# Kernel optimization log

Hardware: AMD Instinct MI355X
Metric: run time of the kernel (lower is better)

The kernel has to match this reference:

```python
import jax, jax.numpy as jnp
import numpy as np

B, T, V, D = 256, 128, 32000, 512
DT = 0.04
CUBIC = 0.008
LAMBDA = 0.1
SIGNAL_SCALE = 0.5
NORM_EPS = 1e-8       # state_norm_eps
SIG_EPS = 1e-6        # signal_eps
SLOW_DECAY = 0.05
SLOW_LR = 0.05
W_FAST = 1.0
W_SLOW = 0.3
CONV_STEPS = 4
LN_EPS = 1e-5


def make_diffusion_matrix(dim):
    rng = np.random.default_rng(42)
    q, _ = np.linalg.qr(rng.standard_normal((dim, dim)).astype(np.float64))
    u = rng.random(dim)
    eig = -0.2 - (0.05 + 0.3 * u)
    return jnp.asarray((q * eig) @ q.T, dtype=jnp.float32)


def setup_inputs() -> dict:
    key = jax.random.key(0)
    k1, k2, k3 = jax.random.split(key, 3)
    tokens = jax.random.randint(k1, (B, T), 0, V)
    embed = jax.random.normal(k2, (V, D), dtype=jnp.float32) * 0.02
    readout_w = jax.random.normal(k3, (V, D), dtype=jnp.float32) * 0.02
    diffusion = make_diffusion_matrix(D)
    gamma = jnp.float32(0.2)
    beta = jnp.float32(0.75)
    return {"tokens": tokens, "embed": embed, "readout_w": readout_w,
            "diffusion": diffusion, "gamma": gamma, "beta": beta}


def _layernorm(x):
    mu = jnp.mean(x, axis=-1, keepdims=True)
    var = jnp.mean((x - mu) ** 2, axis=-1, keepdims=True)
    return (x - mu) / jnp.sqrt(var + LN_EPS)


def _norm(x):
    return jnp.linalg.norm(x, axis=-1, keepdims=True)


def _context_vector(fast, slow):
    combined = W_FAST * fast + W_SLOW * slow
    fn = _norm(fast)
    cn = _norm(combined)
    fast_dir = fast / (fn + SIG_EPS)
    comb_dir = combined / (cn + SIG_EPS)
    return jnp.where(fn > 1e-8, fast_dir,
                     jnp.where(cn > 1e-8, comb_dir, jnp.zeros_like(fast)))


def _step_state(state, signal, diffusion, beta):
    c = state - jnp.mean(state, axis=-1, keepdims=True)
    drift = (state @ diffusion.T + CUBIC * jnp.tanh(c)
             + beta * (SIGNAL_SCALE * signal) - LAMBDA * state)
    s = state + DT * drift
    s = jnp.nan_to_num(s, nan=0.0, posinf=0.0, neginf=0.0)
    s = s / (_norm(s) + NORM_EPS)
    return jnp.clip(s, -10.0, 10.0)


def reference(tokens, embed, readout_w, diffusion, gamma, beta):
    # tokens: [B,T] int; states: [B,D]
    fast0 = jnp.zeros((tokens.shape[0], D), dtype=embed.dtype)
    slow0 = jnp.zeros_like(fast0)

    def token_step(carry, tok):
        fast, slow = carry
        emb = _layernorm(embed[tok])                       # [B,D]
        base = emb / jnp.maximum(_norm(emb), 1e-12)
        ctx = _context_vector(fast, slow)
        sig = base + gamma * ctx
        sig = sig / (_norm(sig) + SIG_EPS)
        for _ in range(CONV_STEPS):
            fast = _step_state(fast, sig, diffusion, beta)
        slow = (1.0 - SLOW_DECAY) * slow + SLOW_LR * fast
        sn = _norm(slow)
        slow = jnp.where(sn > 0.5, slow * (0.5 / (sn + 1e-12)), slow)
        return (fast, slow), None

    (fast, slow), _ = jax.lax.scan(token_step, (fast0, slow0), tokens.T)
    combined = W_FAST * fast + W_SLOW * slow               # [B,D]
    logits = combined @ readout_w.T                        # [B,V]
    return logits
```

## Files before the change

### kernel.cpp

```cpp
#include <hip/hip_runtime.h>
#include <math.h>

#define DDIM 512
#define TLEN 128
#define RB   8
#define NWG  32
#define VDIM 32000
#define NWAVE 8
#define SR   528

typedef _Float16 f16x8 __attribute__((ext_vector_type(8)));
typedef float    f32x4 __attribute__((ext_vector_type(4)));
typedef _Float16 h2    __attribute__((ext_vector_type(2)));

__device__ __forceinline__ unsigned int pkh2(float a, float b) {
  h2 v; v.x = (_Float16)a; v.y = (_Float16)b;
  return __builtin_bit_cast(unsigned int, v);
}
__device__ __forceinline__ float h2f(unsigned short h) {
  return (float)__builtin_bit_cast(_Float16, h);
}
__device__ __forceinline__ unsigned short f2h(float f) {
  return __builtin_bit_cast(unsigned short, (_Float16)f);
}
__device__ __forceinline__ float tanh_fast(float x) {
#if __has_builtin(__builtin_amdgcn_exp2f) && __has_builtin(__builtin_amdgcn_rcpf)
  const float e = __builtin_amdgcn_exp2f(x * 2.885390081777927f);
  return 1.f - 2.f * __builtin_amdgcn_rcpf(e + 1.f);
#else
  const float e = exp2f(x * 2.885390081777927f);
  return 1.f - 2.f / (e + 1.f);
#endif
}
__device__ __forceinline__ f32x4 unpk4(uint2 u) {
  f32x4 r;
  r[0] = h2f((unsigned short)(u.x & 0xffff));
  r[1] = h2f((unsigned short)(u.x >> 16));
  r[2] = h2f((unsigned short)(u.y & 0xffff));
  r[3] = h2f((unsigned short)(u.y >> 16));
  return r;
}

__device__ __forceinline__ void wg_barrier() {
  asm volatile("s_waitcnt lgkmcnt(0)" ::: "memory");
  __builtin_amdgcn_s_barrier();
  asm volatile("" ::: "memory");
}

__global__ __launch_bounds__(256) void pack_diffusion(
    const float* __restrict__ A, uint4* __restrict__ pk)
{
  const int slot = blockIdx.x * 256 + threadIdx.x;
  const int l  = slot & 63;
  const int fr = slot >> 6;
  const int kt = fr & 15;
  const int it = fr >> 4;
  const float* src = A + (size_t)(it * 16 + (l & 15)) * DDIM + kt * 32 + (l >> 4) * 8;
  pk[slot] = make_uint4(pkh2(src[0], src[1]), pkh2(src[2], src[3]),
                        pkh2(src[4], src[5]), pkh2(src[6], src[7]));
}

__global__ __launch_bounds__(512) void precompute_mubi(
    const int*   __restrict__ tokens,
    const float* __restrict__ embed,
    float4*      __restrict__ mubi)
{
  const int idx = blockIdx.x * 8 + (threadIdx.x >> 6);
  const int l   = threadIdx.x & 63;
  const int b   = idx >> 7;
  const int t   = idx & 127;
  const int tok = tokens[b * TLEN + t];
  float s1 = 0.f, s2 = 0.f;
  #pragma unroll
  for (int e = 0; e < 8; ++e) {
    const float v = embed[(size_t)tok * DDIM + l + e * 64];
    s1 += v; s2 += v * v;
  }
  #pragma unroll
  for (int off = 32; off >= 1; off >>= 1) {
    s1 += __shfl_xor(s1, off);
    s2 += __shfl_xor(s2, off);
  }
  if (l == 0) {
    const float mu = s1 * (1.f / DDIM);
    float var = s2 * (1.f / DDIM) - mu * mu;
    var = fmaxf(var, 0.f);
    const float inv  = rsqrtf(var + 1e-5f);
    const float n2y  = (float)DDIM * var / (var + 1e-5f);
    const float invn = 1.f / fmaxf(sqrtf(n2y), 1e-12f);
    mubi[idx] = make_float4(mu, inv * invn, n2y * invn * invn, 0.f);
  }
}

#define USE_AR(KT_)                                                          \
  {                                                                          \
    const f16x8 bf = *(const f16x8*)&srow[rp][rl * SR + (KT_) * 32 + g * 8]; \
    _Pragma("unroll")                                                        \
    for (int mt = 0; mt < 4; ++mt)                                           \
      C[mt] = __builtin_amdgcn_mfma_f32_16x16x32_f16(                        \
          __builtin_bit_cast(f16x8, AR[KT_][mt]), bf, C[mt], 0, 0, 0);       \
  }
#define USE_LD(KT_)                                                          \
  {                                                                          \
    const f16x8 bf = *(const f16x8*)&srow[rp][rl * SR + (KT_) * 32 + g * 8]; \
    _Pragma("unroll")                                                        \
    for (int mt = 0; mt < 4; ++mt) {                                         \
      const uint4 af = ares[((w * 4 + mt) * 4 + ((KT_) - 8)) * 64 + l];      \
      C[mt] = __builtin_amdgcn_mfma_f32_16x16x32_f16(                        \
          __builtin_bit_cast(f16x8, af), bf, C[mt], 0, 0, 0);                \
    }                                                                        \
  }
#define USE_S(J_, KT_)                                                       \
  {                                                                          \
    const f16x8 bf = *(const f16x8*)&srow[rp][rl * SR + (KT_) * 32 + g * 8]; \
    _Pragma("unroll")                                                        \
    for (int mt = 0; mt < 4; ++mt)                                           \
      C[mt] = __builtin_amdgcn_mfma_f32_16x16x32_f16(                        \
          __builtin_bit_cast(f16x8, S##J_[mt]), bf, C[mt], 0, 0, 0);         \
  }
#define PF_S(J_, KT_)                                                        \
  {                                                                          \
    _Pragma("unroll")                                                        \
    for (int mt = 0; mt < 4; ++mt)                                           \
      S##J_[mt] = apw[(size_t)(mt * 16 + (KT_)) * 64];                       \
  }

__global__ __launch_bounds__(512, 1) void attractor_recurrence(
    const int*    __restrict__ tokens,
    const float*  __restrict__ embed,
    const uint4*  __restrict__ Apk,
    const float4* __restrict__ mubi,
    const float*  __restrict__ gamma_p,
    const float*  __restrict__ beta_p,
    float*        __restrict__ comb_out)
{
  const int tid   = threadIdx.x;
  const int w     = tid >> 6;
  const int l     = tid & 63;
  const int g     = l >> 4;
  const int n     = l & 15;
  const int rl    = n & 7;
  const int hi    = (n >> 3) & 1;
  const int row0  = blockIdx.x * RB;
  const int wbase = w * 64;

  __shared__ unsigned short srow[2][RB * SR];
  __shared__ unsigned short forceh[RB * SR];
  __shared__ float4 redc[2][NWAVE][RB];
  __shared__ float4 redt[NWAVE][2];
  __shared__ float2 carry[RB];
  __shared__ float4 mb[RB];
  __shared__ uint4  ares[32 * 4 * 64];

  for (int x = tid; x < RB * SR; x += 512) { srow[0][x] = 0; srow[1][x] = 0; }
  for (int x = tid; x < 32 * 4 * 64; x += 512) {
    const int it = x >> 8;
    const int kr = (x >> 6) & 3;
    const int ll = x & 63;
    ares[x] = Apk[(size_t)(it * 16 + 8 + kr) * 64 + ll];
  }

  const uint4* apw = Apk + (size_t)(w * 64) * 64 + l;
  uint4 AR[8][4];
  #pragma unroll
  for (int kt = 0; kt < 8; ++kt)
    #pragma unroll
    for (int mt = 0; mt < 4; ++mt)
      AR[kt][mt] = apw[(size_t)(mt * 16 + kt) * 64];

  const float gamma = gamma_p[0];
  const float bss   = beta_p[0] * 0.5f;

  float fs[2][4];
  float sl[2][4];
  #pragma unroll
  for (int mtl = 0; mtl < 2; ++mtl)
    #pragma unroll
    for (int q = 0; q < 4; ++q) { fs[mtl][q] = 0.f; sl[mtl][q] = 0.f; }
  float S_reg = 0.f, S2_reg = 0.f, SX_reg = 0.f;
  float sl2 = 0.f;

  float evc[8];
  #pragma unroll
  for (int r = 0; r < 8; ++r) {
    const int tok = tokens[(row0 + r) * TLEN + 0];
    evc[r] = embed[(size_t)tok * DDIM + tid];
  }

  __syncthreads();

  uint4 S0[4], S1[4], S2[4], S3[4];
  PF_S(0, 12); PF_S(1, 13); PF_S(2, 14); PF_S(3, 15);

  for (int t = 0; t < TLEN; ++t) {
    const int tn = (t + 1 < TLEN) ? t + 1 : t;
    float evn[8];
    #pragma unroll
    for (int r = 0; r < 8; ++r) {
      const int tok = tokens[(row0 + r) * TLEN + tn];
      evn[r] = embed[(size_t)tok * DDIM + tid];
    }
    if (tid < 8) mb[tid] = mubi[(size_t)(row0 + tid) * TLEN + t];
    float pr[8];
    #pragma unroll
    for (int r = 0; r < 8; ++r)
      pr[r] = evc[r] * h2f(srow[0][r * SR + tid]);
    #pragma unroll
    for (int off = 32; off >= 1; off >>= 1)
      #pragma unroll
      for (int q = 0; q < 8; ++q)
        pr[q] += __shfl_xor(pr[q], off);
    if (l == 0) {
      redt[w][0] = make_float4(pr[0], pr[1], pr[2], pr[3]);
      redt[w][1] = make_float4(pr[4], pr[5], pr[6], pr[7]);
    }
    if (tid < 8) carry[tid] = make_float2(S_reg, S2_reg);
    if (t > 0) {
      const float sq3   = sqrtf(S2_reg);
      const float ispn3 = 1.f / (sq3 + 1e-8f);
      const float fn3   = sq3 * ispn3;
      const float sdf   = SX_reg * ispn3;
      const float sn2   = 0.9025f * sl2 + 0.095f * sdf + 0.0025f * fn3 * fn3;
      const float sn    = sqrtf(fmaxf(sn2, 0.f));
      const float scale = (sn > 0.5f) ? 0.5f / (sn + 1e-12f) : 1.f;
      sl2 = sn2 * scale * scale;
      #pragma unroll
      for (int mtl = 0; mtl < 2; ++mtl)
        #pragma unroll
        for (int q = 0; q < 4; ++q)
          sl[mtl][q] = (0.95f * sl[mtl][q] + 0.05f * fs[mtl][q] * ispn3) * scale;
    }
    wg_barrier();

    {
      float rs[8];
      #pragma unroll
      for (int q = 0; q < 8; ++q) rs[q] = 0.f;
      #pragma unroll
      for (int wv = 0; wv < NWAVE; ++wv) {
        const float4 v0 = redt[wv][0];
        const float4 v1 = redt[wv][1];
        rs[0] += v0.x; rs[1] += v0.y; rs[2] += v0.z; rs[3] += v0.w;
        rs[4] += v1.x; rs[5] += v1.y; rs[6] += v1.z; rs[7] += v1.w;
      }
      #pragma unroll
      for (int r = 0; r < 8; ++r) {
        const float2 cy  = carry[r];
        const float4 mbr = mb[r];
        const float sq   = sqrtf(cy.y);
        const float ispr = 1.f / (sq + 1e-8f);
        const float fno  = sq * ispr;
        const float invf = 1.f / (fno + 1e-6f);
        const float qr   = ispr * invf;
        const float sctx = qr * cy.x;
        const float bdot = mbr.y * (qr * rs[r] - mbr.x * sctx);
        const float cn2  = qr * qr * cy.y;
        const float sg2  = mbr.z + 2.f * gamma * bdot + gamma * gamma * cn2;
        const float isig = 1.f / (sqrtf(fmaxf(sg2, 0.f)) + 1e-6f);
        const float ctx  = qr * h2f(srow[0][r * SR + tid]);
        forceh[r * SR + tid] = f2h(bss * ((evc[r] - mbr.x) * mbr.y + gamma * ctx) * isig);
      }
    }
    wg_barrier();

    #pragma unroll 1
    for (int k = 0; k < 4; ++k) {
      const int  rp   = k & 1;
      const int  wp   = rp ^ 1;
      const bool last = (k == 3);

      f32x4 C[4];
      #pragma unroll
      for (int mt = 0; mt < 4; ++mt) C[mt] = (f32x4){0.f, 0.f, 0.f, 0.f};

      USE_AR(0); USE_AR(1); USE_AR(2); USE_AR(3);
      USE_AR(4); USE_AR(5); USE_AR(6); USE_AR(7);
      USE_LD(8); USE_LD(9); USE_LD(10); USE_LD(11);
      USE_S(0, 12); USE_S(1, 13); USE_S(2, 14); USE_S(3, 15);
      PF_S(0, 12); PF_S(1, 13); PF_S(2, 14); PF_S(3, 15);

      const float ispn  = 1.f / (sqrtf(S2_reg) + 1e-8f);
      const float smean = S_reg * ispn * (1.f / DDIM);
      f32x4 Cs[2];
      Cs[0] = hi ? C[2] : C[0];
      Cs[1] = hi ? C[3] : C[1];
      const int i0base = wbase + hi * 32 + g * 4;
      float vs = 0.f, v2 = 0.f, vx = 0.f;
      #pragma unroll
      for (int mtl = 0; mtl < 2; ++mtl) {
        const int i0 = i0base + mtl * 16;
        const f32x4 ff = unpk4(*(const uint2*)&forceh[rl * SR + i0]);
        #pragma unroll
        for (int q = 0; q < 4; ++q) {
          const float s   = fs[mtl][q] * ispn;
          const float th  = tanh_fast(s - smean);
          const float dr  = Cs[mtl][q] * ispn + 0.008f * th + ff[q] - 0.1f * s;
          const float spv = fmaf(0.04f, dr, s);
          fs[mtl][q] = spv;
          vs += spv; v2 += spv * spv;
          if (last) vx += sl[mtl][q] * spv;
        }
      }
      vs += __shfl_xor(vs, 8);  v2 += __shfl_xor(v2, 8);  vx += __shfl_xor(vx, 8);
      vs += __shfl_xor(vs, 16); v2 += __shfl_xor(v2, 16); vx += __shfl_xor(vx, 16);
      vs += __shfl_xor(vs, 32); v2 += __shfl_xor(v2, 32); vx += __shfl_xor(vx, 32);

      #pragma unroll
      for (int mtl = 0; mtl < 2; ++mtl) {
        const int i0 = i0base + mtl * 16;
        uint2 pkv;
        pkv.x = pkh2(fs[mtl][0], fs[mtl][1]);
        pkv.y = pkh2(fs[mtl][2], fs[mtl][3]);
        *(uint2*)&srow[wp][rl * SR + i0] = pkv;
      }
      if (l < 8) redc[rp][w][l] = make_float4(vs, v2, vx, 0.f);
      wg_barrier();
      float S = 0.f, S2 = 0.f, SX = 0.f;
      #pragma unroll
      for (int wv = 0; wv < NWAVE; ++wv) {
        const float4 v = redc[rp][wv][rl];
        S += v.x; S2 += v.y; SX += v.z;
      }
      S_reg = S; S2_reg = S2; SX_reg = SX;
    }

    #pragma unroll
    for (int r = 0; r < 8; ++r) evc[r] = evn[r];
  }

  {
    const float sq3   = sqrtf(S2_reg);
    const float ispn3 = 1.f / (sq3 + 1e-8f);
    const float fn3   = sq3 * ispn3;
    const float sdf   = SX_reg * ispn3;
    const float sn2   = 0.9025f * sl2 + 0.095f * sdf + 0.0025f * fn3 * fn3;
    const float sn    = sqrtf(fmaxf(sn2, 0.f));
    const float scale = (sn > 0.5f) ? 0.5f / (sn + 1e-12f) : 1.f;
    const int i0base = wbase + hi * 32 + g * 4;
    #pragma unroll
    for (int mtl = 0; mtl < 2; ++mtl) {
      const int i0 = i0base + mtl * 16;
      float4 o;
      #pragma unroll
      for (int q = 0; q < 4; ++q) {
        const float f = fs[mtl][q] * ispn3;
        const float s = (0.95f * sl[mtl][q] + 0.05f * f) * scale;
        ((float*)&o)[q] = f + 0.3f * s;
      }
      *(float4*)&comb_out[(size_t)(row0 + rl) * DDIM + i0] = o;
    }
  }
}

#define KC  32
#define LDT 132

__global__ __launch_bounds__(256) void logits_gemm(
    const float* __restrict__ comb,
    const float* __restrict__ W,
    float*       __restrict__ out)
{
  __shared__ float wt[KC * LDT];
  __shared__ float ct[KC * LDT];

  const int tid = threadIdx.x;
  const int v0  = blockIdx.x * 128;
  const int b0  = blockIdx.y * 128;
  const int tb  = tid >> 4;
  const int tv  = tid & 15;

  float acc[8][8];
  #pragma unroll
  for (int a = 0; a < 8; ++a)
    #pragma unroll
    for (int b = 0; b < 8; ++b) acc[a][b] = 0.f;

  for (int kk = 0; kk < DDIM; kk += KC) {
    #pragma unroll
    for (int it = 0; it < 4; ++it) {
      const int l4  = tid + it * 256;
      const int row = l4 >> 3;
      const int k4  = (l4 & 7) << 2;
      const float4 gw = *(const float4*)&W[(size_t)(v0 + row) * DDIM + kk + k4];
      const float4 gc = *(const float4*)&comb[(size_t)(b0 + row) * DDIM + kk + k4];
      wt[(k4 + 0) * LDT + row] = gw.x;
      wt[(k4 + 1) * LDT + row] = gw.y;
      wt[(k4 + 2) * LDT + row] = gw.z;
      wt[(k4 + 3) * LDT + row] = gw.w;
      ct[(k4 + 0) * LDT + row] = gc.x;
      ct[(k4 + 1) * LDT + row] = gc.y;
      ct[(k4 + 2) * LDT + row] = gc.z;
      ct[(k4 + 3) * LDT + row] = gc.w;
    }
    __syncthreads();

    for (int kx = 0; kx < KC; ++kx) {
      const float4 c0 = *(const float4*)&ct[kx * LDT + tb * 8];
      const float4 c1 = *(const float4*)&ct[kx * LDT + tb * 8 + 4];
      const float4 w0 = *(const float4*)&wt[kx * LDT + tv * 8];
      const float4 w1 = *(const float4*)&wt[kx * LDT + tv * 8 + 4];
      const float cw[8] = {c0.x, c0.y, c0.z, c0.w, c1.x, c1.y, c1.z, c1.w};
      const float wv[8] = {w0.x, w0.y, w0.z, w0.w, w1.x, w1.y, w1.z, w1.w};
      #pragma unroll
      for (int ib = 0; ib < 8; ++ib)
        #pragma unroll
        for (int iv = 0; iv < 8; ++iv)
          acc[ib][iv] = fmaf(cw[ib], wv[iv], acc[ib][iv]);
    }
    __syncthreads();
  }

  #pragma unroll
  for (int ib = 0; ib < 8; ++ib) {
    const size_t base = (size_t)(b0 + tb * 8 + ib) * VDIM + v0 + tv * 8;
    *(float4*)&out[base]     = make_float4(acc[ib][0], acc[ib][1], acc[ib][2], acc[ib][3]);
    *(float4*)&out[base + 4] = make_float4(acc[ib][4], acc[ib][5], acc[ib][6], acc[ib][7]);
  }
}

extern "C" void kernel_launch(void* const* d_in, const int* in_sizes, int n_in,
                              void* d_out, int out_size, void* d_ws, size_t ws_size,
                              hipStream_t stream) {
  const int*   tokens    = (const int*)d_in[0];
  const float* embed     = (const float*)d_in[1];
  const float* readout_w = (const float*)d_in[2];
  const float* diffusion = (const float*)d_in[3];
  const float* gamma_p   = (const float*)d_in[4];
  const float* beta_p    = (const float*)d_in[5];

  float*  comb = (float*)d_ws;
  uint4*  Apk  = (uint4*)((char*)d_ws + 512 * 1024);
  float4* mubi = (float4*)((char*)d_ws + 1024 * 1024);

  hipLaunchKernelGGL(pack_diffusion, dim3(128), dim3(256), 0, stream,
                     diffusion, Apk);
  hipLaunchKernelGGL(precompute_mubi, dim3(256 * TLEN / 8), dim3(512), 0, stream,
                     tokens, embed, mubi);
  hipLaunchKernelGGL(attractor_recurrence, dim3(NWG), dim3(512), 0, stream,
                     tokens, embed, Apk, mubi, gamma_p, beta_p, comb);
  hipLaunchKernelGGL(logits_gemm, dim3(VDIM / 128, 256 / 128), dim3(256), 0, stream,
                     comb, readout_w, (float*)d_out);
}
```

Measured before the change: 3.847 ms.

## Stream diffusion matrix tiles through rotating register buffers instead of resident registers

Removes the 32 register-resident A-tile fragments (k-tiles 0-7) and instead keeps k-tiles 0-3 in LDS and streams k-tiles 4-15 from global/L2 through a three-deep rotating register buffer that prefetches three steps ahead. This frees many VGPRs and replaces the single bulk prefetch of the last four tiles with a software pipeline interleaved with the MFMAs. The cost is far more global loads per step (12 of 16 k-tiles fetched every convergence step instead of 4), so performance depends on L2 latency being hidden by the prefetch distance.

```diff
diff --git a/kernel.cpp b/kernel.cpp
--- a/kernel.cpp
+++ b/kernel.cpp
@@ -92,37 +92,29 @@
   }
 }
 
-#define USE_AR(KT_)                                                          \
+#define USE_LD(KT_)                                                          \
+  {                                                                          \
+    const f16x8 bf = *(const f16x8*)&srow[rp][rl * SR + (KT_) * 32 + g * 8]; \
+    _Pragma("unroll")                                                        \
+    for (int mt = 0; mt < 4; ++mt) {                                         \
+      const uint4 af = ares[((w * 4 + mt) * 4 + (KT_)) * 64 + l];            \
+      C[mt] = __builtin_amdgcn_mfma_f32_16x16x32_f16(                        \
+          __builtin_bit_cast(f16x8, af), bf, C[mt], 0, 0, 0);                \
+    }                                                                        \
+  }
+#define USE(B_, KT_)                                                         \
   {                                                                          \
     const f16x8 bf = *(const f16x8*)&srow[rp][rl * SR + (KT_) * 32 + g * 8]; \
     _Pragma("unroll")                                                        \
     for (int mt = 0; mt < 4; ++mt)                                           \
       C[mt] = __builtin_amdgcn_mfma_f32_16x16x32_f16(                        \
-          __builtin_bit_cast(f16x8, AR[KT_][mt]), bf, C[mt], 0, 0, 0);       \
-  }
-#define USE_LD(KT_)                                                          \
-  {                                                                          \
-    const f16x8 bf = *(const f16x8*)&srow[rp][rl * SR + (KT_) * 32 + g * 8]; \
-    _Pragma("unroll")                                                        \
-    for (int mt = 0; mt < 4; ++mt) {                                         \
-      const uint4 af = ares[((w * 4 + mt) * 4 + ((KT_) - 8)) * 64 + l];      \
-      C[mt] = __builtin_amdgcn_mfma_f32_16x16x32_f16(                        \
-          __builtin_bit_cast(f16x8, af), bf, C[mt], 0, 0, 0);                \
-    }                                                                        \
-  }
-#define USE_S(J_, KT_)                                                       \
-  {                                                                          \
-    const f16x8 bf = *(const f16x8*)&srow[rp][rl * SR + (KT_) * 32 + g * 8]; \
-    _Pragma("unroll")                                                        \
-    for (int mt = 0; mt < 4; ++mt)                                           \
-      C[mt] = __builtin_amdgcn_mfma_f32_16x16x32_f16(                        \
-          __builtin_bit_cast(f16x8, S##J_[mt]), bf, C[mt], 0, 0, 0);         \
-  }
-#define PF_S(J_, KT_)                                                        \
+          __builtin_bit_cast(f16x8, B_[mt]), bf, C[mt], 0, 0, 0);            \
+  }
+#define PF(B_, KT_)                                                          \
   {                                                                          \
     _Pragma("unroll")                                                        \
     for (int mt = 0; mt < 4; ++mt)                                           \
-      S##J_[mt] = apw[(size_t)(mt * 16 + (KT_)) * 64];                       \
+      B_[mt] = apw[(size_t)(mt * 16 + (KT_)) * 64];                          \
   }
 
 __global__ __launch_bounds__(512, 1) void attractor_recurrence(
@@ -157,16 +149,10 @@
     const int it = x >> 8;
     const int kr = (x >> 6) & 3;
     const int ll = x & 63;
-    ares[x] = Apk[(size_t)(it * 16 + 8 + kr) * 64 + ll];
+    ares[x] = Apk[(size_t)(it * 16 + kr) * 64 + ll];
   }
 
   const uint4* apw = Apk + (size_t)(w * 64) * 64 + l;
-  uint4 AR[8][4];
-  #pragma unroll
-  for (int kt = 0; kt < 8; ++kt)
-    #pragma unroll
-    for (int mt = 0; mt < 4; ++mt)
-      AR[kt][mt] = apw[(size_t)(mt * 16 + kt) * 64];
 
   const float gamma = gamma_p[0];
   const float bss   = beta_p[0] * 0.5f;
@@ -189,8 +175,8 @@
 
   __syncthreads();
 
-  uint4 S0[4], S1[4], S2[4], S3[4];
-  PF_S(0, 12); PF_S(1, 13); PF_S(2, 14); PF_S(3, 15);
+  uint4 A0[4], A1[4], A2[4];
+  PF(A0, 4); PF(A1, 5); PF(A2, 6);
 
   for (int t = 0; t < TLEN; ++t) {
     const int tn = (t + 1 < TLEN) ? t + 1 : t;
@@ -273,11 +259,19 @@
       #pragma unroll
       for (int mt = 0; mt < 4; ++mt) C[mt] = (f32x4){0.f, 0.f, 0.f, 0.f};
 
-      USE_AR(0); USE_AR(1); USE_AR(2); USE_AR(3);
-      USE_AR(4); USE_AR(5); USE_AR(6); USE_AR(7);
-      USE_LD(8); USE_LD(9); USE_LD(10); USE_LD(11);
-      USE_S(0, 12); USE_S(1, 13); USE_S(2, 14); USE_S(3, 15);
-      PF_S(0, 12); PF_S(1, 13); PF_S(2, 14); PF_S(3, 15);
+      USE_LD(0); USE_LD(1); USE_LD(2); USE_LD(3);
+      USE(A0,  4); PF(A0,  7);
+      USE(A1,  5); PF(A1,  8);
+      USE(A2,  6); PF(A2,  9);
+      USE(A0,  7); PF(A0, 10);
+      USE(A1,  8); PF(A1, 11);
+      USE(A2,  9); PF(A2, 12);
+      USE(A0, 10); PF(A0, 13);
+      USE(A1, 11); PF(A1, 14);
+      USE(A2, 12); PF(A2, 15);
+      USE(A0, 13); PF(A0,  4);
+      USE(A1, 14); PF(A1,  5);
+      USE(A2, 15); PF(A2,  6);
 
       const float ispn  = 1.f / (sqrtf(S2_reg) + 1e-8f);
       const float smean = S_reg * ispn * (1.f / DDIM);
```

Measured after the change: 4.239 ms. 10.2% more time.
